# Performance work log

Hardware: AMD Instinct MI355X
Metric: run time of the kernel (lower is better)

The kernel has to match this reference:

```python
import jax, jax.numpy as jnp
import numpy as np

D_MODEL, N_LAYERS, NUM_CLASSES = 768, 4, 10
D_INNER = 2 * D_MODEL          # expand_factor=2
D_STATE = 16
D_CONV = 4
DT_RANK = (D_MODEL + 15) // 16  # ceil(d_model/16) = 48
B, L = 8, 2048
EPS = 1e-5


def setup_inputs() -> dict:
    key = jax.random.key(0)
    ks = jax.random.split(key, 16)
    s = 0.02
    inp = {
        'x': jax.random.normal(ks[0], (B, L, D_MODEL), jnp.float32),
        'labels': jax.random.randint(ks[1], (B,), 0, NUM_CLASSES, jnp.int64),
        # stacked per-layer params
        'in_proj_w': jax.random.normal(ks[2], (N_LAYERS, 2 * D_INNER, D_MODEL), jnp.float32) * s,
        'conv_w': jax.random.normal(ks[3], (N_LAYERS, D_INNER, 1, D_CONV), jnp.float32) * s,
        'conv_b': jnp.zeros((N_LAYERS, D_INNER), jnp.float32),
        'x_proj_w': jax.random.normal(ks[4], (N_LAYERS, DT_RANK + 2 * D_STATE, D_INNER), jnp.float32) * s,
        'dt_w': jax.random.normal(ks[5], (N_LAYERS, D_INNER, DT_RANK), jnp.float32) * s,
        'dt_b': jax.random.uniform(ks[6], (N_LAYERS, D_INNER), jnp.float32, -4.0, -2.0),
        'A_log': jnp.broadcast_to(jnp.log(jnp.arange(1, D_STATE + 1, dtype=jnp.float32)),
                                  (N_LAYERS, D_INNER, D_STATE)).copy(),
        'D_param': jnp.ones((N_LAYERS, D_INNER), jnp.float32),
        'out_proj_w': jax.random.normal(ks[7], (N_LAYERS, D_MODEL, D_INNER), jnp.float32) * s,
        'norm_w': jnp.ones((N_LAYERS, D_MODEL), jnp.float32),
        'normf_w': jnp.ones((D_MODEL,), jnp.float32),
        'cls_w': jax.random.normal(ks[8], (NUM_CLASSES, D_MODEL), jnp.float32) * s,
        'cls_b': jnp.zeros((NUM_CLASSES,), jnp.float32),
    }
    return inp


def rmsnorm(x, w):
    return x * jax.lax.rsqrt(jnp.mean(x * x, axis=-1, keepdims=True) + EPS) * w


def causal_dw_conv1d(x, w, b):
    # x: (B, L, ED), w: (ED, 1, K) depthwise, causal left padding
    y = jax.lax.conv_general_dilated(
        x.swapaxes(1, 2), w, window_strides=(1,), padding=[(D_CONV - 1, 0)],
        feature_group_count=D_INNER, dimension_numbers=('NCH', 'OIH', 'NCH'))
    return (y + b[:, None]).swapaxes(1, 2)


def selective_scan(xin, delta, Bm, Cm, A, Dp):
    # xin/delta: (B,L,ED), Bm/Cm: (B,L,N), A: (ED,N), Dp: (ED,)
    def step(h, t):
        d_t, B_t, C_t, x_t = t                      # (B,ED),(B,N),(B,N),(B,ED)
        dA = jnp.exp(d_t[..., None] * A)            # (B,ED,N)
        dBx = (d_t * x_t)[..., None] * B_t[:, None, :]
        h = dA * h + dBx
        y = jnp.einsum('ben,bn->be', h, C_t)
        return h, y

    h0 = jnp.zeros((xin.shape[0], D_INNER, D_STATE), xin.dtype)
    xs = (delta.swapaxes(0, 1), Bm.swapaxes(0, 1), Cm.swapaxes(0, 1), xin.swapaxes(0, 1))
    _, ys = jax.lax.scan(step, h0, xs)              # ys: (L,B,ED)
    return ys.swapaxes(0, 1) + xin * Dp


def mamba_block(x, in_w, cw, cb, xw, dtw, dtb, A_log, Dp, ow):
    xz = jnp.einsum('bld,ed->ble', x, in_w)         # (B,L,2*ED)
    xin, z = jnp.split(xz, 2, axis=-1)
    xin = jax.nn.silu(causal_dw_conv1d(xin, cw, cb))
    dbc = jnp.einsum('ble,fe->blf', xin, xw)
    delta_r = dbc[..., :DT_RANK]
    Bm = dbc[..., DT_RANK:DT_RANK + D_STATE]
    Cm = dbc[..., DT_RANK + D_STATE:]
    delta = jax.nn.softplus(jnp.einsum('blr,er->ble', delta_r, dtw) + dtb)
    A = -jnp.exp(A_log)
    y = selective_scan(xin, delta, Bm, Cm, A, Dp)
    y = y * jax.nn.silu(z)
    return jnp.einsum('ble,de->bld', y, ow)


def forward(x, labels, in_proj_w, conv_w, conv_b, x_proj_w, dt_w, dt_b,
            A_log, D_param, out_proj_w, norm_w, normf_w, cls_w, cls_b):
    h = x
    for i in range(N_LAYERS):
        h = h + mamba_block(rmsnorm(h, norm_w[i]), in_proj_w[i], conv_w[i], conv_b[i],
                            x_proj_w[i], dt_w[i], dt_b[i], A_log[i], D_param[i], out_proj_w[i])
    h = rmsnorm(h, normf_w)
    pooled = jnp.mean(h, axis=1)                    # (B, d_model)
    logits = pooled @ cls_w.T + cls_b               # (B, num_classes)
    logp = jax.nn.log_softmax(logits, axis=-1)
    loss = -jnp.mean(jnp.take_along_axis(logp, labels[:, None], axis=-1))
    return logits, loss


def reference(x, labels, in_proj_w, conv_w, conv_b, x_proj_w, dt_w, dt_b,
              A_log, D_param, out_proj_w, norm_w, normf_w, cls_w, cls_b):
    return forward(x, labels, in_proj_w, conv_w, conv_b, x_proj_w, dt_w, dt_b,
                   A_log, D_param, out_proj_w, norm_w, normf_w, cls_w, cls_b)
```

## Files before the change

kernel.cpp:

```cpp
#include <hip/hip_runtime.h>
#include <hip/hip_bf16.h>
#include <math.h>

#define MTOK 16384
#define DM   768
#define DI   1536
#define DS   16
#define RNK  48
#define LSEQ 2048
#define NBATCH 8
#define EPSV 1e-5f
#define CHK  16
#define CLEN (LSEQ / CHK)
#define BM 128
#define BN 128
#define BK 32
#define KSPLIT 8
#define EPS_STRIDE 72

typedef __hip_bfloat16 bf16;
typedef __attribute__((ext_vector_type(8))) short short8;
typedef __attribute__((ext_vector_type(4))) float floatx4;

__device__ __forceinline__ float b2f(bf16 v){ return __bfloat162float(v); }
__device__ __forceinline__ bf16  f2b(float v){ return __float2bfloat16(v); }
__device__ __forceinline__ float u2f(unsigned short u){
    union { unsigned int i; float f; } v; v.i = ((unsigned int)u) << 16; return v.f;
}
__device__ __forceinline__ unsigned pack_bf2(float a, float b){
    bf16 ta = f2b(a), tb = f2b(b);
    return (unsigned)(*(unsigned short*)&ta) | ((unsigned)(*(unsigned short*)&tb) << 16);
}
__device__ __forceinline__ float silu_f(float x){
    return x * __builtin_amdgcn_rcpf(1.f + __expf(-x));
}
__device__ __forceinline__ void gload_lds16(const void* g, void* l) {
    __builtin_amdgcn_global_load_lds(
        (const __attribute__((address_space(1))) void*)g,
        (__attribute__((address_space(3))) void*)l, 16, 0, 0);
}

__global__ __launch_bounds__(256) void cvt_kernel(
    const float* __restrict__ x, bf16* __restrict__ h, int n)
{
    int i = (blockIdx.x * 256 + threadIdx.x) * 4;
    if (i < n) {
        const float4 v = *(const float4*)(x + i);
        uint2 o;
        o.x = pack_bf2(v.x, v.y);
        o.y = pack_bf2(v.z, v.w);
        *(uint2*)((unsigned short*)h + i) = o;
    }
}

__global__ __launch_bounds__(256) void rmsnorm_kernel(
    const bf16* __restrict__ in, const float* __restrict__ w,
    bf16* __restrict__ out, float* __restrict__ rs_out)
{
    const int row  = blockIdx.x * 4 + (threadIdx.x >> 6);
    const int lane = threadIdx.x & 63;
    const unsigned short* rp = (const unsigned short*)in + (size_t)row * DM + lane * 12;
    uint2 u0 = *(const uint2*)rp;
    uint2 u1 = *(const uint2*)(rp + 4);
    uint2 u2 = *(const uint2*)(rp + 8);
    unsigned us[6] = {u0.x, u0.y, u1.x, u1.y, u2.x, u2.y};
    float v[12];
    #pragma unroll
    for (int i = 0; i < 6; i++) {
        v[2*i]   = u2f((unsigned short)(us[i] & 0xffff));
        v[2*i+1] = u2f((unsigned short)(us[i] >> 16));
    }
    float s = 0.f;
    #pragma unroll
    for (int i = 0; i < 12; i++) s += v[i] * v[i];
    #pragma unroll
    for (int o = 32; o > 0; o >>= 1) s += __shfl_xor(s, o, 64);
    float rs = rsqrtf(s * (1.f/DM) + EPSV);
    if (rs_out && lane == 0) rs_out[row] = rs;
    if (out) {
        const float4 w0 = *(const float4*)(w + lane*12);
        const float4 w1 = *(const float4*)(w + lane*12 + 4);
        const float4 w2 = *(const float4*)(w + lane*12 + 8);
        unsigned short* op = (unsigned short*)out + (size_t)row * DM + lane * 12;
        uint2 o0, o1, o2;
        o0.x = pack_bf2(v[0]*rs*w0.x,  v[1]*rs*w0.y);
        o0.y = pack_bf2(v[2]*rs*w0.z,  v[3]*rs*w0.w);
        o1.x = pack_bf2(v[4]*rs*w1.x,  v[5]*rs*w1.y);
        o1.y = pack_bf2(v[6]*rs*w1.z,  v[7]*rs*w1.w);
        o2.x = pack_bf2(v[8]*rs*w2.x,  v[9]*rs*w2.y);
        o2.y = pack_bf2(v[10]*rs*w2.z, v[11]*rs*w2.w);
        *(uint2*)op       = o0;
        *(uint2*)(op + 4) = o1;
        *(uint2*)(op + 8) = o2;
    }
}

template<int MODE>
__global__ __launch_bounds__(256) void mgemm(
    const short* __restrict__ A, int lda,
    const short* __restrict__ W, int ldw,
    bf16* __restrict__ C, int ldc,
    int M, int N, int K)
{
    __shared__ __attribute__((aligned(16))) short lds[3 * 8192];

    const int gx = gridDim.x;
    int lid = blockIdx.y * gx + blockIdx.x;
    {
        const int nwg = gx * gridDim.y;
        const int q = nwg >> 3, r = nwg & 7;
        const int xcd = lid & 7, slot = lid >> 3;
        lid = (xcd < r ? xcd * (q + 1) : r * (q + 1) + (xcd - r) * q) + slot;
    }
    const int bm = (lid / gx) * BM;
    const int bn = (lid % gx) * BN;

    const int tid = threadIdx.x;
    const int wave = tid >> 6;
    const int lane = tid & 63;
    const int wm = (wave & 1) * 64;
    const int wn = (wave >> 1) * 64;
    const int r15 = lane & 15;
    const int quad = lane >> 4;

    const int srow = wave*32 + (lane >> 2);
    const int swz = (lane & 3) ^ ((lane >> 3) & 3);
    int wr0 = bn + srow;      if (wr0 >= N) wr0 = N - 1;
    int wr1 = bn + srow + 16; if (wr1 >= N) wr1 = N - 1;

    const short* Ab  = A + (size_t)(bm + srow) * lda + swz*8;
    const short* Ab1 = A + (size_t)(bm + srow + 16) * lda + swz*8;
    const short* Wb0 = W + (size_t)wr0 * ldw + swz*8;
    const short* Wb1 = W + (size_t)wr1 * ldw + swz*8;
    const int dA0 = (wave*32)*BK;
    const int dA1 = (wave*32 + 16)*BK;
    const int dB0 = 4096 + (wave*32)*BK;
    const int dB1 = 4096 + (wave*32 + 16)*BK;

    floatx4 acc[4][4];
    const floatx4 zero = {0.f, 0.f, 0.f, 0.f};
    #pragma unroll
    for (int i = 0; i < 4; i++)
        #pragma unroll
        for (int j = 0; j < 4; j++) acc[i][j] = zero;

    const int sA = quad ^ ((r15 >> 1) & 3);
    const int sB = sA;

    const int NK = K / BK;

    auto STAGE = [&](int buf, int kt) {
        const int bb = buf * 8192;
        const size_t kc = (size_t)kt * BK;
        gload_lds16(Ab  + kc, &lds[bb + dA0]);
        gload_lds16(Ab1 + kc, &lds[bb + dA1]);
        gload_lds16(Wb0 + kc, &lds[bb + dB0]);
        gload_lds16(Wb1 + kc, &lds[bb + dB1]);
    };

    STAGE(0, 0); STAGE(1, 1);
    asm volatile("s_waitcnt vmcnt(4)" ::: "memory");
    __builtin_amdgcn_s_barrier();
    __builtin_amdgcn_sched_barrier(0);

    for (int t = 0; t < NK; ++t) {
        const short* As = &lds[(t % 3) * 8192];
        const short* Bs = As + 4096;

        short8 af[4], bfr[4];
        #pragma unroll
        for (int i = 0; i < 4; i++) af[i]  = *(const short8*)&As[(wm + i*16 + r15)*BK + sA*8];
        #pragma unroll
        for (int i = 0; i < 4; i++) bfr[i] = *(const short8*)&Bs[(wn + i*16 + r15)*BK + sB*8];

        if (t + 2 < NK) STAGE((t + 2) % 3, t + 2);

        __builtin_amdgcn_s_setprio(1);
        #pragma unroll
        for (int mt = 0; mt < 4; mt++)
            #pragma unroll
            for (int nt = 0; nt < 4; nt++)
                acc[mt][nt] = __builtin_amdgcn_mfma_f32_16x16x32_bf16(
                    af[mt], bfr[nt], acc[mt][nt], 0, 0, 0);
        __builtin_amdgcn_s_setprio(0);

        if (t + 2 < NK)      asm volatile("s_waitcnt vmcnt(4)" ::: "memory");
        else if (t + 1 < NK) asm volatile("s_waitcnt vmcnt(0)" ::: "memory");
        __builtin_amdgcn_s_barrier();
        __builtin_amdgcn_sched_barrier(0);
    }

    short* ep = lds + ((wave & 2) ? 4096 : 0) + (wave & 1) * 1152;
    const int lr = lane >> 2;
    const int lc = lane & 3;
    #pragma unroll
    for (int mt = 0; mt < 4; mt++) {
        #pragma unroll
        for (int nt = 0; nt < 4; nt++)
            #pragma unroll
            for (int reg = 0; reg < 4; reg++) {
                bf16 t = f2b(acc[mt][nt][reg]);
                ep[(quad*4 + reg)*EPS_STRIDE + nt*16 + r15] = *(short*)&t;
            }
        short8 v0 = *(const short8*)&ep[lr*EPS_STRIDE + lc*16];
        short8 v1 = *(const short8*)&ep[lr*EPS_STRIDE + lc*16 + 8];
        int gm = bm + wm + mt*16 + lr;
        int gn = bn + wn + lc*16;
        if (gn < N) {
            bf16* cp = C + (size_t)gm * ldc + gn;
            if (MODE == 0) {
                *(short8*)cp       = v0;
                *(short8*)(cp + 8) = v1;
            } else {
                short8 c0 = *(const short8*)cp;
                short8 c1 = *(const short8*)(cp + 8);
                short8 o0, o1;
                #pragma unroll
                for (int j = 0; j < 8; j++) {
                    float cv0 = u2f((unsigned short)c0[j]);
                    float av0 = u2f((unsigned short)v0[j]);
                    float cv1 = u2f((unsigned short)c1[j]);
                    float av1 = u2f((unsigned short)v1[j]);
                    float r0 = (MODE == 2) ? (cv0 + av0) : (cv0 * silu_f(av0));
                    float r1 = (MODE == 2) ? (cv1 + av1) : (cv1 * silu_f(av1));
                    bf16 t0 = f2b(r0), t1 = f2b(r1);
                    o0[j] = *(short*)&t0;
                    o1[j] = *(short*)&t1;
                }
                *(short8*)cp       = o0;
                *(short8*)(cp + 8) = o1;
            }
        }
    }
}

__global__ __launch_bounds__(256) void mgemm_conv(
    const short* __restrict__ A, int lda,
    const short* __restrict__ W, int ldw,
    float* __restrict__ Cf, int ldc,
    int M, int N, int K,
    const float* __restrict__ cw, const float* __restrict__ cb,
    int ksteps_per_split)
{
    __shared__ __attribute__((aligned(16))) short As[BM*BK];
    __shared__ __attribute__((aligned(16))) short Bs[BN*BK];

    const int gx = gridDim.x;
    int lid = blockIdx.y * gx + blockIdx.x;
    {
        const int nwg = gx * gridDim.y;
        const int q = nwg >> 3, r = nwg & 7;
        const int xcd = lid & 7, slot = lid >> 3;
        lid = (xcd < r ? xcd * (q + 1) : r * (q + 1) + (xcd - r) * q) + slot;
    }
    const int bm = (lid / gx) * BM;
    const int bn = (lid % gx) * BN;

    const int tid = threadIdx.x;
    const int wave = tid >> 6;
    const int lane = tid & 63;
    const int wm = (wave & 1) * 64;
    const int wn = (wave >> 1) * 64;
    const int r15 = lane & 15;
    const int quad = lane >> 4;

    int kbeg = blockIdx.z * ksteps_per_split * BK;
    int kend = kbeg + ksteps_per_split * BK;
    if (kend > K) kend = K;

    const int srow = wave*32 + (lane >> 2);
    const int swz = (lane & 3) ^ ((lane >> 3) & 3);
    int wr0 = bn + srow;      if (wr0 >= N) wr0 = N - 1;
    int wr1 = bn + srow + 16; if (wr1 >= N) wr1 = N - 1;

    floatx4 acc[4][4];
    const floatx4 zero = {0.f, 0.f, 0.f, 0.f};
    #pragma unroll
    for (int i = 0; i < 4; i++)
        #pragma unroll
        for (int j = 0; j < 4; j++) acc[i][j] = zero;

    const int kk = tid & 31;
    const int tg = tid >> 5;
    const int sA = quad;
    const int sB = quad ^ ((r15 >> 1) & 3);

    for (int k0 = kbeg; k0 < kend; k0 += BK) {
        {
            int e = k0 + kk;
            float c0 = cw[e*4+0], c1 = cw[e*4+1], c2 = cw[e*4+2], c3 = cw[e*4+3];
            float cbe = cb[e];
            int g0 = bm + tg*16;
            const unsigned short* xp = (const unsigned short*)A + (size_t)g0 * lda + e;
            float p0 = 0.f, p1 = 0.f, p2 = 0.f;
            if ((g0 & (LSEQ-1)) != 0) {
                p0 = u2f(xp[-(ptrdiff_t)3*lda]);
                p1 = u2f(xp[-(ptrdiff_t)2*lda]);
                p2 = u2f(xp[-(ptrdiff_t)1*lda]);
            }
            #pragma unroll
            for (int i = 0; i < 16; i++) {
                float xt = u2f(xp[(size_t)i * lda]);
                float xv = silu_f(cbe + c0*p0 + c1*p1 + c2*p2 + c3*xt);
                p0 = p1; p1 = p2; p2 = xt;
                bf16 t = f2b(xv);
                As[(tg*16 + i)*BK + kk] = *(short*)&t;
            }
        }
        gload_lds16(W + (size_t)wr0 * ldw + k0 + swz*8, &Bs[(wave*32)*BK]);
        gload_lds16(W + (size_t)wr1 * ldw + k0 + swz*8, &Bs[(wave*32 + 16)*BK]);
        __syncthreads();

        short8 af[4], bfr[4];
        #pragma unroll
        for (int i = 0; i < 4; i++) af[i]  = *(const short8*)&As[(wm + i*16 + r15)*BK + sA*8];
        #pragma unroll
        for (int i = 0; i < 4; i++) bfr[i] = *(const short8*)&Bs[(wn + i*16 + r15)*BK + sB*8];
        #pragma unroll
        for (int mt = 0; mt < 4; mt++)
            #pragma unroll
            for (int nt = 0; nt < 4; nt++)
                acc[mt][nt] = __builtin_amdgcn_mfma_f32_16x16x32_bf16(
                    af[mt], bfr[nt], acc[mt][nt], 0, 0, 0);
        __syncthreads();
    }

    #pragma unroll
    for (int nt = 0; nt < 4; nt++) {
        int n = bn + wn + nt*16 + r15;
        if (n >= N) continue;
        #pragma unroll
        for (int mt = 0; mt < 4; mt++)
            #pragma unroll
            for (int reg = 0; reg < 4; reg++) {
                int m = bm + wm + mt*16 + quad*4 + reg;
                atomicAdd(&Cf[(size_t)m * ldc + n], acc[mt][nt][reg]);
            }
    }
}

template<int PASS>
__global__ __launch_bounds__(256) void scan_pass_kernel(
    bf16* __restrict__ xy, int xld, int gate,
    const bf16* __restrict__ dbc,
    const float* __restrict__ A_log,
    const float* __restrict__ Dp,
    const float* __restrict__ dtw,
    const float* __restrict__ dtb,
    const float* __restrict__ cw,
    const float* __restrict__ cb,
    float* __restrict__ hst,
    float* __restrict__ Ssum,
    unsigned short* __restrict__ bound)
{
    int e = (blockIdx.x % (DI/256)) * 256 + threadIdx.x;
    int b = (blockIdx.x / (DI/256)) & (NBATCH - 1);
    int c = blockIdx.x / ((DI/256) * NBATCH);
    int t0 = c * CLEN;

    float w[RNK];
    #pragma unroll
    for (int r = 0; r < RNK; r++) w[r] = dtw[e*RNK + r];
    float a[DS];
    #pragma unroll
    for (int n = 0; n < DS; n++) a[n] = -__expf(A_log[e*DS + n]);
    float c0 = cw[e*4+0], c1 = cw[e*4+1], c2 = cw[e*4+2], c3 = cw[e*4+3];
    float cbe = cb[e], dtbe = dtb[e], dpe = Dp[e];

    size_t sidx = ((size_t)(b*DI) + e) * CHK + c;
    float hh[DS];
    if (PASS == 1) {
        #pragma unroll
        for (int n = 0; n < DS; n++) hh[n] = 0.f;
    } else {
        #pragma unroll
        for (int n = 0; n < DS; n++) hh[n] = hst[sidx*DS + n];
    }

    unsigned short* xrow = (unsigned short*)xy + ((size_t)(b*LSEQ) + t0) * xld + e;
    const unsigned short* drow = (const unsigned short*)(dbc + ((size_t)(b*LSEQ) + t0) * 80);

    unsigned short r0, r1, r2;
    if (PASS == 1) {
        if (c == 0) { r0 = 0; r1 = 0; r2 = 0; }
        else {
            r0 = xrow[-(ptrdiff_t)3*xld];
            r1 = xrow[-(ptrdiff_t)2*xld];
            r2 = xrow[-(ptrdiff_t)1*xld];
        }
        bound[sidx*4+0] = r0; bound[sidx*4+1] = r1; bound[sidx*4+2] = r2;
    } else {
        r0 = bound[sidx*4+0]; r1 = bound[sidx*4+1]; r2 = bound[sidx*4+2];
    }
    float p0 = u2f(r0), p1 = u2f(r1), p2 = u2f(r2);

    float S = 0.f;
    for (int t = 0; t < CLEN; t++) {
        float xt = u2f(xrow[(size_t)t * xld]);
        float xv = silu_f(cbe + c0*p0 + c1*p1 + c2*p2 + c3*xt);
        p0 = p1; p1 = p2; p2 = xt;

        uint4 q[5];
        const uint4* d4 = (const uint4*)(drow + (size_t)t * 80);
        #pragma unroll
        for (int i = 0; i < 5; i++) q[i] = d4[i];
        uint4 q2[5];
        #pragma unroll
        for (int i = 0; i < 5; i++) q2[i] = d4[5 + i];
        const unsigned short* ds = (const unsigned short*)q;
        const unsigned short* ds2 = (const unsigned short*)q2;

        float acc = dtbe;
        #pragma unroll
        for (int r = 0; r < RNK; r++) acc += w[r] * u2f(ds[r]);
        float d = (acc > 20.f) ? acc : __logf(1.f + __expf(acc));
        float dx = d * xv;
        #pragma unroll
        for (int n = 0; n < DS; n++)
            hh[n] = __expf(d * a[n]) * hh[n] + dx * u2f(ds[RNK + n]);

        if (PASS == 1) {
            S += d;
        } else {
            float y = xv * dpe;
            #pragma unroll
            for (int n = 0; n < DS; n++) y += hh[n] * u2f(ds2[n]);
            if (gate) {
                float zt = u2f(xrow[(size_t)t * xld + 1536]);
                y *= silu_f(zt);
            }
            bf16 yb = f2b(y);
            xrow[(size_t)t * xld] = *(unsigned short*)&yb;
        }
    }
    if (PASS == 1) {
        #pragma unroll
        for (int n = 0; n < DS; n++) hst[sidx*DS + n] = hh[n];
        Ssum[sidx] = S;
    }
}

__global__ __launch_bounds__(256) void scan_combine_kernel(
    float* __restrict__ hst, const float* __restrict__ Ssum,
    const float* __restrict__ A_log)
{
    int tid = blockIdx.x * 256 + threadIdx.x;
    int n = tid & 15;
    int bee = tid >> 4;
    int e = bee % DI;
    float a = -__expf(A_log[e*DS + n]);
    float run = 0.f;
    for (int c = 0; c < CHK; c++) {
        size_t idx = ((size_t)bee * CHK + c) * DS + n;
        float tmp = hst[idx];
        hst[idx] = run;
        run = tmp + __expf(a * Ssum[(size_t)bee*CHK + c]) * run;
    }
}

__global__ __launch_bounds__(128) void pool_kernel(
    const bf16* __restrict__ h, const float* __restrict__ rs,
    const float* __restrict__ wf, float* __restrict__ pooled)
{
    int b = blockIdx.x, dc = blockIdx.y, tc = blockIdx.z;
    int d = dc * 128 + threadIdx.x;
    float s = 0.f;
    int t0 = tc * 128;
    for (int t = t0; t < t0 + 128; t++) {
        int row = b * LSEQ + t;
        s += b2f(h[(size_t)row * DM + d]) * rs[row];
    }
    atomicAdd(&pooled[b * DM + d], s * wf[d] * (1.f / LSEQ));
}

__global__ __launch_bounds__(128) void head_kernel(
    const float* __restrict__ pooled, const float* __restrict__ cls_w,
    const float* __restrict__ cls_b, const int* __restrict__ labels,
    float* __restrict__ out)
{
    __shared__ float lg[80];
    int tid = threadIdx.x;
    if (tid < 80) {
        int b = tid / 10, c = tid % 10;
        float s = cls_b[c];
        for (int d = 0; d < DM; d++) s += pooled[b * DM + d] * cls_w[c * DM + d];
        lg[tid] = s;
    }
    __syncthreads();
    if (tid == 0) {
        float loss = 0.f;
        for (int b = 0; b < NBATCH; b++) {
            float mx = -1e30f;
            for (int c = 0; c < 10; c++) mx = fmaxf(mx, lg[b*10+c]);
            float se = 0.f;
            for (int c = 0; c < 10; c++) se += expf(lg[b*10+c] - mx);
            float lse = mx + logf(se);
            loss -= (lg[b*10 + labels[b]] - lse);
            for (int c = 0; c < 10; c++) out[b*10+c] = lg[b*10+c];
        }
        out[80] = loss / NBATCH;
    }
}

extern "C" void kernel_launch(void* const* d_in, const int* in_sizes, int n_in,
                              void* d_out, int out_size, void* d_ws, size_t ws_size,
                              hipStream_t stream) {
    const float* x          = (const float*)d_in[0];
    const int*   labels     = (const int*)d_in[1];
    const float* in_proj_w  = (const float*)d_in[2];
    const float* conv_w     = (const float*)d_in[3];
    const float* conv_b     = (const float*)d_in[4];
    const float* x_proj_w   = (const float*)d_in[5];
    const float* dt_w       = (const float*)d_in[6];
    const float* dt_b       = (const float*)d_in[7];
    const float* A_log      = (const float*)d_in[8];
    const float* D_param    = (const float*)d_in[9];
    const float* out_proj_w = (const float*)d_in[10];
    const float* norm_w     = (const float*)d_in[11];
    const float* normf_w    = (const float*)d_in[12];
    const float* cls_w      = (const float*)d_in[13];
    const float* cls_b      = (const float*)d_in[14];
    float* out = (float*)d_out;

    const size_t fixed = (size_t)MTOK*DM*2*2
                       + (size_t)MTOK*80*2 + (size_t)MTOK*80*4
                       + (size_t)NBATCH*DI*CHK*DS*4 + (size_t)NBATCH*DI*CHK*4
                       + (size_t)NBATCH*DI*CHK*4*2
                       + (size_t)MTOK*4 + (size_t)NBATCH*DM*4
                       + (size_t)2*DI*DM*2 + (size_t)80*DI*2 + (size_t)DM*DI*2;
    const int fused = (ws_size >= fixed + (size_t)MTOK * (2*DI) * 2 + 1024) ? 1 : 0;
    const int XLD = fused ? 2*DI : DI;

    char* p = (char*)d_ws;
    bf16* h   = (bf16*)p;                 p += (size_t)MTOK * DM * 2;
    bf16* xn  = (bf16*)p;                 p += (size_t)MTOK * DM * 2;
    bf16* xz  = (bf16*)p;                 p += (size_t)MTOK * XLD * 2;
    bf16* dbc = (bf16*)p;                 p += (size_t)MTOK * 80 * 2;
    float* dbcf = (float*)p;              p += (size_t)MTOK * 80 * 4;
    float* hst = (float*)p;               p += (size_t)NBATCH*DI*CHK*DS*4;
    float* Ssum = (float*)p;              p += (size_t)NBATCH*DI*CHK*4;
    unsigned short* bound = (unsigned short*)p; p += (size_t)NBATCH*DI*CHK*4*2;
    float* rsb    = (float*)p;            p += (size_t)MTOK * 4;
    float* pooled = (float*)p;            p += NBATCH * DM * 4;
    short* inw_b = (short*)p;             p += (size_t)2*DI*DM * 2;
    short* xw_b  = (short*)p;             p += (size_t)80*DI * 2;
    short* ow_b  = (short*)p;             p += (size_t)DM*DI * 2;

    cvt_kernel<<<(MTOK * DM) / 1024, 256, 0, stream>>>(x, h, MTOK * DM);
    hipMemsetAsync(pooled, 0, NBATCH * DM * sizeof(float), stream);

    int scan_grid = (DI/256) * NBATCH * CHK;

    for (int l = 0; l < 4; l++) {
        const float* inw = in_proj_w + (size_t)l * 2 * DI * DM;
        const float* cwl = conv_w + (size_t)l * DI * 4;
        const float* cbl = conv_b + (size_t)l * DI;
        const float* xwl = x_proj_w + (size_t)l * (RNK + 2*DS) * DI;
        const float* dwl = dt_w + (size_t)l * DI * RNK;
        const float* dbl = dt_b + (size_t)l * DI;
        const float* All = A_log + (size_t)l * DI * DS;
        const float* Dpl = D_param + (size_t)l * DI;
        const float* owl = out_proj_w + (size_t)l * DM * DI;

        cvt_kernel<<<(2*DI*DM)/1024, 256, 0, stream>>>(inw, (bf16*)inw_b, 2*DI*DM);
        cvt_kernel<<<(80*DI)/1024, 256, 0, stream>>>(xwl, (bf16*)xw_b, 80*DI);
        cvt_kernel<<<(DM*DI)/1024, 256, 0, stream>>>(owl, (bf16*)ow_b, DM*DI);

        rmsnorm_kernel<<<MTOK/4, 256, 0, stream>>>(h, norm_w + (size_t)l * DM, xn, nullptr);

        hipMemsetAsync(dbcf, 0, (size_t)MTOK * 80 * sizeof(float), stream);

        if (fused) {
            mgemm<0><<<dim3(2*DI/BN, MTOK/BM), 256, 0, stream>>>(
                (const short*)xn, DM, inw_b, DM, xz, XLD, MTOK, 2*DI, DM);
        } else {
            mgemm<0><<<dim3(DI/BN, MTOK/BM), 256, 0, stream>>>(
                (const short*)xn, DM, inw_b, DM, xz, XLD, MTOK, DI, DM);
        }

        mgemm_conv<<<dim3(1, MTOK/BM, KSPLIT), 256, 0, stream>>>(
            (const short*)xz, XLD, xw_b, DI, dbcf, 80, MTOK, 80, DI,
            cwl, cbl, (DI/BK)/KSPLIT);
        cvt_kernel<<<(MTOK*80)/1024, 256, 0, stream>>>(dbcf, dbc, MTOK*80);

        scan_pass_kernel<1><<<scan_grid, 256, 0, stream>>>(
            xz, XLD, 0, dbc, All, Dpl, dwl, dbl, cwl, cbl, hst, Ssum, bound);
        scan_combine_kernel<<<(NBATCH*DI*DS)/256, 256, 0, stream>>>(hst, Ssum, All);
        scan_pass_kernel<2><<<scan_grid, 256, 0, stream>>>(
            xz, XLD, fused, dbc, All, Dpl, dwl, dbl, cwl, cbl, hst, Ssum, bound);

        if (!fused) {
            mgemm<3><<<dim3(DI/BN, MTOK/BM), 256, 0, stream>>>(
                (const short*)xn, DM, inw_b + (size_t)DI*DM, DM, xz, XLD, MTOK, DI, DM);
        }

        mgemm<2><<<dim3(DM/BN, MTOK/BM), 256, 0, stream>>>(
            (const short*)xz, XLD, ow_b, DI, h, DM, MTOK, DM, DI);
    }

    rmsnorm_kernel<<<MTOK/4, 256, 0, stream>>>(h, normf_w, nullptr, rsb);
    pool_kernel<<<dim3(NBATCH, DM/128, LSEQ/128), 128, 0, stream>>>(h, rsb, normf_w, pooled);
    head_kernel<<<1, 128, 0, stream>>>(pooled, cls_w, cls_b, labels, out);
}
```

Baseline: 1.113 ms.

## Use power-chain decay when A equals -(n+1) and remap GEMM tiles per XCD

The scan kernel now checks at runtime whether A = -exp(A_log) equals -(n+1) for every state. If it does, it computes exp(d*a[n]) as successive powers of exp(-d), replacing sixteen exponentials per step with one exponential and fifteen multiplies. It falls back to the generic path otherwise. The GEMM also gets a new workgroup-to-tile mapping that assigns contiguous row bands to each XCD, with column chunks of 12, to improve L2 reuse. The fast path is specialised to the test's A_log initialisation and gives slightly different rounding through the repeated multiplication.

```diff
diff --git a/kernel.cpp b/kernel.cpp
--- a/kernel.cpp
+++ b/kernel.cpp
@@ -105,15 +105,25 @@
     __shared__ __attribute__((aligned(16))) short lds[3 * 8192];
 
     const int gx = gridDim.x;
-    int lid = blockIdx.y * gx + blockIdx.x;
-    {
-        const int nwg = gx * gridDim.y;
+    const int lid0 = blockIdx.y * gx + blockIdx.x;
+    const int nwg = gx * gridDim.y;
+    int bm, bn;
+    const int nper = nwg >> 3;
+    if ((nwg & 7) == 0 && nper % gx == 0) {
+        const int xcd = lid0 & 7, s = lid0 >> 3;
+        const int Rx = nper / gx;
+        const int CW = (gx % 12 == 0) ? 12 : gx;
+        const int ch = s / (Rx * CW);
+        const int rem = s - ch * (Rx * CW);
+        bm = (xcd * Rx + rem / CW) * BM;
+        bn = (ch * CW + rem % CW) * BN;
+    } else {
         const int q = nwg >> 3, r = nwg & 7;
-        const int xcd = lid & 7, slot = lid >> 3;
-        lid = (xcd < r ? xcd * (q + 1) : r * (q + 1) + (xcd - r) * q) + slot;
-    }
-    const int bm = (lid / gx) * BM;
-    const int bn = (lid % gx) * BN;
+        const int xcd = lid0 & 7, slot = lid0 >> 3;
+        int lid = (xcd < r ? xcd * (q + 1) : r * (q + 1) + (xcd - r) * q) + slot;
+        bm = (lid / gx) * BM;
+        bn = (lid % gx) * BN;
+    }
 
     const int tid = threadIdx.x;
     const int wave = tid >> 6;
@@ -364,6 +374,10 @@
     float a[DS];
     #pragma unroll
     for (int n = 0; n < DS; n++) a[n] = -__expf(A_log[e*DS + n]);
+    bool fast = true;
+    #pragma unroll
+    for (int n = 0; n < DS; n++)
+        fast = fast && (fabsf(a[n] + (float)(n + 1)) <= 1e-4f * (float)(n + 1));
     float c0 = cw[e*4+0], c1 = cw[e*4+1], c2 = cw[e*4+2], c3 = cw[e*4+3];
     float cbe = cb[e], dtbe = dtb[e], dpe = Dp[e];
 
@@ -395,44 +409,51 @@
     float p0 = u2f(r0), p1 = u2f(r1), p2 = u2f(r2);
 
     float S = 0.f;
-    for (int t = 0; t < CLEN; t++) {
-        float xt = u2f(xrow[(size_t)t * xld]);
-        float xv = silu_f(cbe + c0*p0 + c1*p1 + c2*p2 + c3*xt);
-        p0 = p1; p1 = p2; p2 = xt;
-
-        uint4 q[5];
-        const uint4* d4 = (const uint4*)(drow + (size_t)t * 80);
-        #pragma unroll
-        for (int i = 0; i < 5; i++) q[i] = d4[i];
-        uint4 q2[5];
-        #pragma unroll
-        for (int i = 0; i < 5; i++) q2[i] = d4[5 + i];
-        const unsigned short* ds = (const unsigned short*)q;
-        const unsigned short* ds2 = (const unsigned short*)q2;
-
-        float acc = dtbe;
-        #pragma unroll
-        for (int r = 0; r < RNK; r++) acc += w[r] * u2f(ds[r]);
-        float d = (acc > 20.f) ? acc : __logf(1.f + __expf(acc));
-        float dx = d * xv;
-        #pragma unroll
-        for (int n = 0; n < DS; n++)
-            hh[n] = __expf(d * a[n]) * hh[n] + dx * u2f(ds[RNK + n]);
-
-        if (PASS == 1) {
-            S += d;
-        } else {
-            float y = xv * dpe;
-            #pragma unroll
-            for (int n = 0; n < DS; n++) y += hh[n] * u2f(ds2[n]);
-            if (gate) {
-                float zt = u2f(xrow[(size_t)t * xld + 1536]);
-                y *= silu_f(zt);
-            }
-            bf16 yb = f2b(y);
-            xrow[(size_t)t * xld] = *(unsigned short*)&yb;
-        }
-    }
+
+#define SCAN_BODY(FAST_)                                                      \
+    for (int t = 0; t < CLEN; t++) {                                          \
+        float xt = u2f(xrow[(size_t)t * xld]);                                \
+        float xv = silu_f(cbe + c0*p0 + c1*p1 + c2*p2 + c3*xt);               \
+        p0 = p1; p1 = p2; p2 = xt;                                            \
+        uint4 q[5];                                                           \
+        const uint4* d4 = (const uint4*)(drow + (size_t)t * 80);              \
+        _Pragma("unroll") for (int i = 0; i < 5; i++) q[i] = d4[i];           \
+        uint4 q2[5];                                                          \
+        _Pragma("unroll") for (int i = 0; i < 5; i++) q2[i] = d4[5 + i];      \
+        const unsigned short* ds = (const unsigned short*)q;                  \
+        const unsigned short* ds2 = (const unsigned short*)q2;                \
+        float acc = dtbe;                                                     \
+        _Pragma("unroll") for (int r = 0; r < RNK; r++) acc += w[r] * u2f(ds[r]); \
+        float d = (acc > 20.f) ? acc : __logf(1.f + __expf(acc));             \
+        float dx = d * xv;                                                    \
+        if (FAST_) {                                                          \
+            float rp = __expf(-d);                                            \
+            float pw = rp;                                                    \
+            _Pragma("unroll") for (int n = 0; n < DS; n++) {                  \
+                hh[n] = pw * hh[n] + dx * u2f(ds[RNK + n]);                   \
+                pw *= rp;                                                     \
+            }                                                                 \
+        } else {                                                              \
+            _Pragma("unroll") for (int n = 0; n < DS; n++)                    \
+                hh[n] = __expf(d * a[n]) * hh[n] + dx * u2f(ds[RNK + n]);     \
+        }                                                                     \
+        if (PASS == 1) {                                                      \
+            S += d;                                                           \
+        } else {                                                              \
+            float y = xv * dpe;                                               \
+            _Pragma("unroll") for (int n = 0; n < DS; n++) y += hh[n] * u2f(ds2[n]); \
+            if (gate) {                                                       \
+                float zt = u2f(xrow[(size_t)t * xld + 1536]);                 \
+                y *= silu_f(zt);                                              \
+            }                                                                 \
+            bf16 yb = f2b(y);                                                 \
+            xrow[(size_t)t * xld] = *(unsigned short*)&yb;                    \
+        }                                                                     \
+    }
+
+    if (fast) { SCAN_BODY(1) } else { SCAN_BODY(0) }
+#undef SCAN_BODY
+
     if (PASS == 1) {
         #pragma unroll
         for (int n = 0; n < DS; n++) hst[sidx*DS + n] = hh[n];
```

New measurement: 1.103 ms. About the same (-0.9%).
